# Kernel optimization log

Measured on AMD Instinct MI355X. Metric: run time of the kernel, lower is better.

Reference implementation:

```python
import jax, jax.numpy as jnp
import numpy as np

B, T, C, H = 4, 4096, 1024, 128

def setup_inputs() -> dict:
    key = jax.random.key(0)
    kx, kk, kq, kv = jax.random.split(key, 4)
    x = jax.random.normal(kx, (B, T, C), dtype=jnp.float32)
    # torch nn.Linear(C, H, bias=False) stored here as [C, H] so y = x @ W
    s = 1.0 / np.sqrt(C)
    w_key = jax.random.uniform(kk, (C, H), jnp.float32, -s, s)
    w_query = jax.random.uniform(kq, (C, H), jnp.float32, -s, s)
    w_value = jax.random.uniform(kv, (C, H), jnp.float32, -s, s)
    return {"x": x, "w_key": w_key, "w_query": w_query, "w_value": w_value}

def reference(x, w_key, w_query, w_value):
    # Single-head causal self-attention (dropout p=0.0 -> identity).
    k = x @ w_key      # [B,T,H]
    q = x @ w_query    # [B,T,H]
    v = x @ w_value    # [B,T,H]
    scale = k.shape[-1] ** -0.5
    scores = jnp.einsum('bqh,bkh->bqk', q, k) * scale  # [B,T,T]
    causal = jnp.tril(jnp.ones((x.shape[1], x.shape[1]), dtype=bool))
    scores = jnp.where(causal, scores, -jnp.inf)
    attn = jax.nn.softmax(scores, axis=-1)
    return jnp.einsum('bqk,bkh->bqh', attn, v)  # [B,T,H]
```

## Files before the change

### kernel.cpp

```cpp
#include <hip/hip_runtime.h>
#include <hip/hip_bf16.h>


typedef unsigned short u16;
typedef __attribute__((ext_vector_type(8))) __bf16 bf16x8;
typedef __attribute__((ext_vector_type(8))) u16 u16x8;
typedef __attribute__((ext_vector_type(4))) u16 u16x4;
typedef __attribute__((ext_vector_type(4))) float f32x4;

#define T_DIM 4096
#define C_DIM 1024
#define H_DIM 128
#define EPB 272
#define WS_SPLIT_NEED 50135040ull

static __device__ __forceinline__ f32x4 mfma16x16(u16x8 a, u16x8 b, f32x4 c) {
  return __builtin_amdgcn_mfma_f32_16x16x32_bf16(
      __builtin_bit_cast(bf16x8, a), __builtin_bit_cast(bf16x8, b), c, 0, 0, 0);
}

static __device__ __forceinline__ u16 f2bf(float f) {
  __hip_bfloat16 h = __float2bfloat16(f);
  return __builtin_bit_cast(u16, h);
}

static __device__ __forceinline__ float bf2f(u16 u) {
  unsigned x = (unsigned)u << 16;
  return __builtin_bit_cast(float, x);
}

static __device__ __forceinline__ void gll16(const u16* g, u16* l) {
  __builtin_amdgcn_global_load_lds(
      (const __attribute__((address_space(1))) void*)(void*)g,
      (__attribute__((address_space(3))) void*)l, 16, 0, 0);
}

__global__ __launch_bounds__(256) void prep_w_kernel(
    const float* __restrict__ wk, const float* __restrict__ wq,
    const float* __restrict__ wv, u16* __restrict__ Wf) {
  const int oid = blockIdx.x * 256 + threadIdx.x;
  const int w = oid >> 14;
  const int r = oid & 16383;
  const int nb = r >> 11;
  const int kb = (r >> 6) & 31;
  const int lane = r & 63;
  const int g = lane >> 4, lq = lane & 15;
  const float* W = (w == 0) ? wk : (w == 1) ? wq : wv;
  const float sc = (w == 1) ? 0.08838834764831845f : 1.0f;
  const int k0 = kb * 32 + g * 8;
  const int n = nb * 16 + lq;
  u16x8 o;
#pragma unroll
  for (int j = 0; j < 8; ++j) o[j] = f2bf(W[(size_t)(k0 + j) * H_DIM + n] * sc);
  *(u16x8*)&Wf[(size_t)oid * 8] = o;
}

__global__ __launch_bounds__(512, 2) void proj_kernel(
    const float* __restrict__ x, const u16* __restrict__ Wf,
    u16* __restrict__ Qb, u16* __restrict__ Kb, u16* __restrict__ Vt) {
  __shared__ __attribute__((aligned(16))) u16 smem[32 * 1024];
  const int m0 = blockIdx.x * 32;
  const int t = threadIdx.x;
  const int wave = t >> 6, lane = t & 63;
  const int g = lane >> 4, lq = lane & 15;
  const int lsw = lq & 7;

#pragma unroll
  for (int p = 0; p < 8; ++p) {
    int c = p * 512 + t;
    int row = c >> 7, cc = c & 127;
    const float* xp = &x[(size_t)(m0 + row) * C_DIM + cc * 8];
    float4 v0 = *(const float4*)xp;
    float4 v1 = *(const float4*)(xp + 4);
    u16x8 bv;
    bv[0] = f2bf(v0.x); bv[1] = f2bf(v0.y); bv[2] = f2bf(v0.z); bv[3] = f2bf(v0.w);
    bv[4] = f2bf(v1.x); bv[5] = f2bf(v1.y); bv[6] = f2bf(v1.z); bv[7] = f2bf(v1.w);
    *(u16x8*)&smem[row * 1024 + ((cc ^ (row & 7)) * 8)] = bv;
  }
  __syncthreads();

  f32x4 acc[2][3] = {};
  const u16* wfp[3];
#pragma unroll
  for (int j = 0; j < 3; ++j)
    wfp[j] = &Wf[(size_t)((wave * 3 + j) * 32) * 512 + lane * 8];

  u16x8 bcur[3], bnxt[3];
#pragma unroll
  for (int j = 0; j < 3; ++j) bcur[j] = *(const u16x8*)wfp[j];

  for (int kb = 0; kb < 32; ++kb) {
    const int kn = (kb + 1) & 31;
#pragma unroll
    for (int j = 0; j < 3; ++j)
      bnxt[j] = *(const u16x8*)(wfp[j] + (size_t)kn * 512);
    u16x8 af[2];
#pragma unroll
    for (int i = 0; i < 2; ++i)
      af[i] = *(const u16x8*)&smem[(i * 16 + lq) * 1024 +
                                   (((kb * 4 + g) ^ lsw) * 8)];
#pragma unroll
    for (int i = 0; i < 2; ++i)
#pragma unroll
      for (int j = 0; j < 3; ++j)
        acc[i][j] = mfma16x16(af[i], bcur[j], acc[i][j]);
#pragma unroll
    for (int j = 0; j < 3; ++j) bcur[j] = bnxt[j];
  }

#pragma unroll
  for (int j = 0; j < 3; ++j) {
    const int c384 = wave * 48 + j * 16;
    const int which = c384 >> 7;
    const int col = (c384 & 127) + lq;
    if (which == 0) {
#pragma unroll
      for (int i = 0; i < 2; ++i)
#pragma unroll
        for (int r = 0; r < 4; ++r)
          Kb[(size_t)(m0 + i * 16 + g * 4 + r) * H_DIM + col] =
              f2bf(acc[i][j][r]);
    } else if (which == 1) {
#pragma unroll
      for (int i = 0; i < 2; ++i)
#pragma unroll
        for (int r = 0; r < 4; ++r)
          Qb[(size_t)(m0 + i * 16 + g * 4 + r) * H_DIM + col] =
              f2bf(acc[i][j][r]);
    }
  }
  __syncthreads();
#pragma unroll
  for (int j = 0; j < 3; ++j) {
    const int c384 = wave * 48 + j * 16;
    if ((c384 >> 7) == 2) {
      const int v = (c384 & 127) + lq;
#pragma unroll
      for (int i = 0; i < 2; ++i)
#pragma unroll
        for (int r = 0; r < 4; ++r)
          smem[v * 40 + i * 16 + g * 4 + r] = f2bf(acc[i][j][r]);
    }
  }
  __syncthreads();
  {
    const int b = m0 >> 12;
    const int t0 = m0 & 4095;
    int h = t >> 2, mc = (t & 3) * 8;
    *(u16x8*)&Vt[(size_t)b * (H_DIM * T_DIM) + (size_t)h * T_DIM + t0 + mc] =
        *(const u16x8*)&smem[h * 40 + mc];
  }
}

__global__ __launch_bounds__(512, 4) void attn_kernel(
    const u16* __restrict__ Qb, const u16* __restrict__ Kb,
    const u16* __restrict__ Vt, float* __restrict__ out,
    u16* __restrict__ Opart, float* __restrict__ ml, int split) {
  __shared__ __attribute__((aligned(16))) u16 Kl[64 * 128];
  __shared__ __attribute__((aligned(16))) u16 Vl[128 * 64];
  __shared__ __attribute__((aligned(16))) u16 Pl[8][16 * 72];
  const int t = threadIdx.x;
  const int wave = t >> 6, lane = t & 63;
  const int g = lane >> 4, lq = lane & 15;
  const int lsw = lane & 7;

  int b, qb, kvb, kve, pid;
  if (split) {
    int bid = (int)blockIdx.x;
    int xcd = bid & 7;
    b = xcd >> 1;
    int e = (EPB - 1) - ((bid >> 3) * 2 + (bid & 1));
    int a = 0;
#pragma unroll
    for (int c = 1; c <= 15; ++c)
      if (e >= c * (c + 1)) a = c;
    int off = e - a * (a + 1);
    int d = off / (a + 1);
    int ch = off - d * (a + 1);
    qb = 2 * a + d;
    kvb = ch * 256;
    pid = b * EPB + e;
    int kv_full = qb * 128 + 128;
    kve = (kvb + 256 < kv_full) ? kvb + 256 : kv_full;
  } else {
    b = (int)blockIdx.x & 3;
    qb = 31 - ((int)blockIdx.x >> 2);
    kvb = 0;
    kve = qb * 128 + 128;
    pid = 0;
  }
  const int rowq = qb * 128 + wave * 16;
  const int qrow = rowq + lq;

  u16x8 qf[4];
  {
    const u16* Qp = Qb + (size_t)(b * T_DIM + qrow) * H_DIM;
#pragma unroll
    for (int c = 0; c < 4; ++c) qf[c] = *(const u16x8*)&Qp[c * 32 + g * 8];
  }

  f32x4 ao[8] = {};
  float m_run = -INFINITY, l_run = 0.f;

  const u16* Kg0 = Kb + (size_t)b * T_DIM * H_DIM;
  const u16* Vg0 = Vt + (size_t)b * H_DIM * T_DIM;

  for (int kv0 = kvb; kv0 < kve; kv0 += 64) {
    __syncthreads();
#pragma unroll
    for (int i = 0; i < 2; ++i) {
      int r0 = (i * 8 + wave) * 4;
      int r = r0 + (lane >> 4);
      int csrc = (lane & 15) ^ (r & 7);
      gll16(&Kg0[(size_t)(kv0 + r) * H_DIM + csrc * 8], &Kl[r0 * 128]);
    }
#pragma unroll
    for (int i = 0; i < 2; ++i) {
      int h0 = (i * 8 + wave) * 8;
      int h = h0 + (lane >> 3);
      int csrc = (lane & 7) ^ (lane >> 3);
      gll16(&Vg0[(size_t)h * T_DIM + kv0 + csrc * 8], &Vl[h0 * 64]);
    }
    __syncthreads();

    if (kv0 > rowq + 15) continue;

    f32x4 s[4];
#pragma unroll
    for (int nf = 0; nf < 4; ++nf) s[nf] = f32x4{0.f, 0.f, 0.f, 0.f};
#pragma unroll
    for (int nf = 0; nf < 4; ++nf)
#pragma unroll
      for (int c = 0; c < 4; ++c) {
        u16x8 kf = *(const u16x8*)&Kl[(nf * 16 + lq) * 128 +
                                      (((c * 4 + g) ^ lsw) * 8)];
        s[nf] = mfma16x16(kf, qf[c], s[nf]);
      }

    if (kv0 + 63 > rowq) {
      const int kb = kv0 + g * 4;
#pragma unroll
      for (int nf = 0; nf < 4; ++nf)
#pragma unroll
        for (int r = 0; r < 4; ++r)
          if (kb + nf * 16 + r > qrow) s[nf][r] = -INFINITY;
    }

    float t0 = fmaxf(fmaxf(s[0][0], s[0][1]), fmaxf(s[0][2], s[0][3]));
    float t1 = fmaxf(fmaxf(s[1][0], s[1][1]), fmaxf(s[1][2], s[1][3]));
    float t2 = fmaxf(fmaxf(s[2][0], s[2][1]), fmaxf(s[2][2], s[2][3]));
    float t3 = fmaxf(fmaxf(s[3][0], s[3][1]), fmaxf(s[3][2], s[3][3]));
    float pmax = fmaxf(fmaxf(t0, t1), fmaxf(t2, t3));
    pmax = fmaxf(pmax, __shfl_xor(pmax, 16));
    pmax = fmaxf(pmax, __shfl_xor(pmax, 32));

    float mn = fmaxf(m_run, pmax);
    float al = __expf(m_run - mn);
    m_run = mn;
#pragma unroll
    for (int nf = 0; nf < 4; ++nf)
#pragma unroll
      for (int r = 0; r < 4; ++r) s[nf][r] = __expf(s[nf][r] - mn);
    float u0 = (s[0][0] + s[0][1]) + (s[0][2] + s[0][3]);
    float u1 = (s[1][0] + s[1][1]) + (s[1][2] + s[1][3]);
    float u2 = (s[2][0] + s[2][1]) + (s[2][2] + s[2][3]);
    float u3 = (s[3][0] + s[3][1]) + (s[3][2] + s[3][3]);
    float ps = (u0 + u1) + (u2 + u3);
    ps += __shfl_xor(ps, 16);
    ps += __shfl_xor(ps, 32);
    l_run = l_run * al + ps;

    if (!__all(al == 1.f)) {
      float alr[4];
#pragma unroll
      for (int r = 0; r < 4; ++r) alr[r] = __shfl(al, g * 4 + r);
#pragma unroll
      for (int h8 = 0; h8 < 8; ++h8)
#pragma unroll
        for (int r = 0; r < 4; ++r) ao[h8][r] *= alr[r];
    }

#pragma unroll
    for (int nf = 0; nf < 4; ++nf) {
      u16x4 pw;
#pragma unroll
      for (int r = 0; r < 4; ++r) pw[r] = f2bf(s[nf][r]);
      *(u16x4*)&Pl[wave][lq * 72 + nf * 16 + g * 4] = pw;
    }

    u16x8 pf[2];
#pragma unroll
    for (int kk = 0; kk < 2; ++kk)
      pf[kk] = *(const u16x8*)&Pl[wave][lq * 72 + kk * 32 + g * 8];
#pragma unroll
    for (int h8 = 0; h8 < 8; ++h8)
#pragma unroll
      for (int kk = 0; kk < 2; ++kk) {
        u16x8 vf = *(const u16x8*)&Vl[(h8 * 16 + lq) * 64 +
                                      (((kk * 4 + g) ^ lsw) * 8)];
        ao[h8] = mfma16x16(pf[kk], vf, ao[h8]);
      }
  }

  if (!split) {
    float linv = 1.f / l_run;
    float inv[4];
#pragma unroll
    for (int r = 0; r < 4; ++r) inv[r] = __shfl(linv, g * 4 + r);
    float* Og = out + (size_t)(b * T_DIM + rowq) * H_DIM;
#pragma unroll
    for (int h8 = 0; h8 < 8; ++h8)
#pragma unroll
      for (int r = 0; r < 4; ++r)
        Og[(size_t)(g * 4 + r) * H_DIM + h8 * 16 + lq] = ao[h8][r] * inv[r];
  } else {
    u16* Op = Opart + (size_t)pid * 16384 + (size_t)(wave * 16) * H_DIM;
#pragma unroll
    for (int h8 = 0; h8 < 8; ++h8)
#pragma unroll
      for (int r = 0; r < 4; ++r)
        Op[(g * 4 + r) * H_DIM + h8 * 16 + lq] = f2bf(ao[h8][r]);
    if (lane < 16) {
      float* mlp = ml + (size_t)pid * 256;
      mlp[wave * 16 + lane] = m_run;
      mlp[128 + wave * 16 + lane] = l_run;
    }
  }
}

__global__ __launch_bounds__(256) void combine_kernel(
    const u16* __restrict__ Opart, const float* __restrict__ ml,
    float* __restrict__ out) {
  const int blk = blockIdx.x;
  const int qb = blk >> 2;
  const int sub = blk & 3;
  const int b = blockIdx.y;
  const int t = threadIdx.x;
  const int row = sub * 32 + (t >> 3);
  const int colb = (t & 7) * 16;
  const int a = qb >> 1;
  const int n = a + 1;
  const int base = a * (a + 1) + (qb & 1) * (a + 1);
  const int pid0 = b * EPB + base;

  float M = -INFINITY;
  for (int i = 0; i < n; ++i)
    M = fmaxf(M, ml[(size_t)(pid0 + i) * 256 + row]);

  float L = 0.f;
  float o[16] = {};
  for (int i = 0; i < n; ++i) {
    const size_t mb = (size_t)(pid0 + i) * 256;
    float sc = __expf(ml[mb + row] - M);
    L += sc * ml[mb + 128 + row];
    const u16* Op = Opart + (size_t)(pid0 + i) * 16384 + row * H_DIM + colb;
#pragma unroll
    for (int p = 0; p < 2; ++p) {
      u16x8 v = *(const u16x8*)&Op[p * 8];
#pragma unroll
      for (int e = 0; e < 8; ++e) o[p * 8 + e] += sc * bf2f(v[e]);
    }
  }
  float inv = 1.f / L;
  float* Og = out + ((size_t)b * T_DIM + qb * 128 + row) * H_DIM + colb;
#pragma unroll
  for (int p = 0; p < 4; ++p) {
    f32x4 v = {o[p * 4] * inv, o[p * 4 + 1] * inv, o[p * 4 + 2] * inv,
               o[p * 4 + 3] * inv};
    *(f32x4*)&Og[p * 4] = v;
  }
}

extern "C" void kernel_launch(void* const* d_in, const int* in_sizes, int n_in,
                              void* d_out, int out_size, void* d_ws,
                              size_t ws_size, hipStream_t stream) {
  const float* x = (const float*)d_in[0];
  const float* wk = (const float*)d_in[1];
  const float* wq = (const float*)d_in[2];
  const float* wv = (const float*)d_in[3];
  float* out = (float*)d_out;
  char* ws = (char*)d_ws;

  u16* Wf = (u16*)ws;
  u16* Qb = (u16*)(ws + 786432);
  u16* Kb = (u16*)(ws + 786432 + 4194304);
  u16* Vt = (u16*)(ws + 786432 + 8388608);
  u16* Opart = (u16*)(ws + 13369344);
  float* ml = (float*)(ws + 49020928);

  const int split = (ws_size >= WS_SPLIT_NEED) ? 1 : 0;

  prep_w_kernel<<<192, 256, 0, stream>>>(wk, wq, wv, Wf);
  proj_kernel<<<512, 512, 0, stream>>>(x, Wf, Qb, Kb, Vt);
  if (split) {
    attn_kernel<<<4 * EPB, 512, 0, stream>>>(Qb, Kb, Vt, out, Opart, ml, 1);
    combine_kernel<<<dim3(128, 4), 256, 0, stream>>>(Opart, ml, out);
  } else {
    attn_kernel<<<128, 512, 0, stream>>>(Qb, Kb, Vt, out, Opart, ml, 0);
  }
}
```

Measured before the change: 84.60 us.

## Process 32 query rows per wave with 4-wave blocks to reuse K/V fragments

```diff
diff --git a/kernel.cpp b/kernel.cpp
--- a/kernel.cpp
+++ b/kernel.cpp
@@ -152,13 +152,13 @@
   }
 }
 
-__global__ __launch_bounds__(512, 4) void attn_kernel(
+__global__ __launch_bounds__(256, 3) void attn_kernel(
     const u16* __restrict__ Qb, const u16* __restrict__ Kb,
     const u16* __restrict__ Vt, float* __restrict__ out,
     u16* __restrict__ Opart, float* __restrict__ ml, int split) {
   __shared__ __attribute__((aligned(16))) u16 Kl[64 * 128];
   __shared__ __attribute__((aligned(16))) u16 Vl[128 * 64];
-  __shared__ __attribute__((aligned(16))) u16 Pl[8][16 * 72];
+  __shared__ __attribute__((aligned(16))) u16 Pl[4][32 * 72];
   const int t = threadIdx.x;
   const int wave = t >> 6, lane = t & 63;
   const int g = lane >> 4, lq = lane & 15;
@@ -189,18 +189,18 @@
     kve = qb * 128 + 128;
     pid = 0;
   }
-  const int rowq = qb * 128 + wave * 16;
-  const int qrow = rowq + lq;
-
-  u16x8 qf[4];
-  {
-    const u16* Qp = Qb + (size_t)(b * T_DIM + qrow) * H_DIM;
-#pragma unroll
-    for (int c = 0; c < 4; ++c) qf[c] = *(const u16x8*)&Qp[c * 32 + g * 8];
-  }
-
-  f32x4 ao[8] = {};
-  float m_run = -INFINITY, l_run = 0.f;
+  const int rowq = qb * 128 + wave * 32;
+
+  u16x8 qf[2][4];
+#pragma unroll
+  for (int rf = 0; rf < 2; ++rf) {
+    const u16* Qp = Qb + (size_t)(b * T_DIM + rowq + rf * 16 + lq) * H_DIM;
+#pragma unroll
+    for (int c = 0; c < 4; ++c) qf[rf][c] = *(const u16x8*)&Qp[c * 32 + g * 8];
+  }
+
+  f32x4 ao[2][8] = {};
+  float m_run[2] = {-INFINITY, -INFINITY}, l_run[2] = {0.f, 0.f};
 
   const u16* Kg0 = Kb + (size_t)b * T_DIM * H_DIM;
   const u16* Vg0 = Vt + (size_t)b * H_DIM * T_DIM;
@@ -208,122 +208,157 @@
   for (int kv0 = kvb; kv0 < kve; kv0 += 64) {
     __syncthreads();
 #pragma unroll
-    for (int i = 0; i < 2; ++i) {
-      int r0 = (i * 8 + wave) * 4;
+    for (int i = 0; i < 4; ++i) {
+      int r0 = (i * 4 + wave) * 4;
       int r = r0 + (lane >> 4);
       int csrc = (lane & 15) ^ (r & 7);
       gll16(&Kg0[(size_t)(kv0 + r) * H_DIM + csrc * 8], &Kl[r0 * 128]);
     }
 #pragma unroll
-    for (int i = 0; i < 2; ++i) {
-      int h0 = (i * 8 + wave) * 8;
+    for (int i = 0; i < 4; ++i) {
+      int h0 = (i * 4 + wave) * 8;
       int h = h0 + (lane >> 3);
       int csrc = (lane & 7) ^ (lane >> 3);
       gll16(&Vg0[(size_t)h * T_DIM + kv0 + csrc * 8], &Vl[h0 * 64]);
     }
     __syncthreads();
 
-    if (kv0 > rowq + 15) continue;
-
-    f32x4 s[4];
-#pragma unroll
-    for (int nf = 0; nf < 4; ++nf) s[nf] = f32x4{0.f, 0.f, 0.f, 0.f};
+    if (kv0 > rowq + 31) continue;
+
+    f32x4 s[2][4];
+#pragma unroll
+    for (int rf = 0; rf < 2; ++rf)
+#pragma unroll
+      for (int nf = 0; nf < 4; ++nf) s[rf][nf] = f32x4{0.f, 0.f, 0.f, 0.f};
 #pragma unroll
     for (int nf = 0; nf < 4; ++nf)
 #pragma unroll
       for (int c = 0; c < 4; ++c) {
         u16x8 kf = *(const u16x8*)&Kl[(nf * 16 + lq) * 128 +
                                       (((c * 4 + g) ^ lsw) * 8)];
-        s[nf] = mfma16x16(kf, qf[c], s[nf]);
+#pragma unroll
+        for (int rf = 0; rf < 2; ++rf)
+          s[rf][nf] = mfma16x16(kf, qf[rf][c], s[rf][nf]);
       }
 
     if (kv0 + 63 > rowq) {
       const int kb = kv0 + g * 4;
 #pragma unroll
+      for (int rf = 0; rf < 2; ++rf) {
+        const int qrow = rowq + rf * 16 + lq;
+#pragma unroll
+        for (int nf = 0; nf < 4; ++nf)
+#pragma unroll
+          for (int r = 0; r < 4; ++r)
+            if (kb + nf * 16 + r > qrow) s[rf][nf][r] = -INFINITY;
+      }
+    }
+
+    float al[2];
+#pragma unroll
+    for (int rf = 0; rf < 2; ++rf) {
+      float t0 = fmaxf(fmaxf(s[rf][0][0], s[rf][0][1]),
+                       fmaxf(s[rf][0][2], s[rf][0][3]));
+      float t1 = fmaxf(fmaxf(s[rf][1][0], s[rf][1][1]),
+                       fmaxf(s[rf][1][2], s[rf][1][3]));
+      float t2 = fmaxf(fmaxf(s[rf][2][0], s[rf][2][1]),
+                       fmaxf(s[rf][2][2], s[rf][2][3]));
+      float t3 = fmaxf(fmaxf(s[rf][3][0], s[rf][3][1]),
+                       fmaxf(s[rf][3][2], s[rf][3][3]));
+      float pmax = fmaxf(fmaxf(t0, t1), fmaxf(t2, t3));
+      pmax = fmaxf(pmax, __shfl_xor(pmax, 16));
+      pmax = fmaxf(pmax, __shfl_xor(pmax, 32));
+      float mn = fmaxf(m_run[rf], pmax);
+      al[rf] = __expf(m_run[rf] - mn);
+      m_run[rf] = mn;
+#pragma unroll
       for (int nf = 0; nf < 4; ++nf)
 #pragma unroll
-        for (int r = 0; r < 4; ++r)
-          if (kb + nf * 16 + r > qrow) s[nf][r] = -INFINITY;
-    }
-
-    float t0 = fmaxf(fmaxf(s[0][0], s[0][1]), fmaxf(s[0][2], s[0][3]));
-    float t1 = fmaxf(fmaxf(s[1][0], s[1][1]), fmaxf(s[1][2], s[1][3]));
-    float t2 = fmaxf(fmaxf(s[2][0], s[2][1]), fmaxf(s[2][2], s[2][3]));
-    float t3 = fmaxf(fmaxf(s[3][0], s[3][1]), fmaxf(s[3][2], s[3][3]));
-    float pmax = fmaxf(fmaxf(t0, t1), fmaxf(t2, t3));
-    pmax = fmaxf(pmax, __shfl_xor(pmax, 16));
-    pmax = fmaxf(pmax, __shfl_xor(pmax, 32));
-
-    float mn = fmaxf(m_run, pmax);
-    float al = __expf(m_run - mn);
-    m_run = mn;
-#pragma unroll
-    for (int nf = 0; nf < 4; ++nf)
-#pragma unroll
-      for (int r = 0; r < 4; ++r) s[nf][r] = __expf(s[nf][r] - mn);
-    float u0 = (s[0][0] + s[0][1]) + (s[0][2] + s[0][3]);
-    float u1 = (s[1][0] + s[1][1]) + (s[1][2] + s[1][3]);
-    float u2 = (s[2][0] + s[2][1]) + (s[2][2] + s[2][3]);
-    float u3 = (s[3][0] + s[3][1]) + (s[3][2] + s[3][3]);
-    float ps = (u0 + u1) + (u2 + u3);
-    ps += __shfl_xor(ps, 16);
-    ps += __shfl_xor(ps, 32);
-    l_run = l_run * al + ps;
-
-    if (!__all(al == 1.f)) {
-      float alr[4];
-#pragma unroll
-      for (int r = 0; r < 4; ++r) alr[r] = __shfl(al, g * 4 + r);
-#pragma unroll
-      for (int h8 = 0; h8 < 8; ++h8)
-#pragma unroll
-        for (int r = 0; r < 4; ++r) ao[h8][r] *= alr[r];
-    }
-
-#pragma unroll
-    for (int nf = 0; nf < 4; ++nf) {
-      u16x4 pw;
-#pragma unroll
-      for (int r = 0; r < 4; ++r) pw[r] = f2bf(s[nf][r]);
-      *(u16x4*)&Pl[wave][lq * 72 + nf * 16 + g * 4] = pw;
-    }
-
-    u16x8 pf[2];
-#pragma unroll
-    for (int kk = 0; kk < 2; ++kk)
-      pf[kk] = *(const u16x8*)&Pl[wave][lq * 72 + kk * 32 + g * 8];
+        for (int r = 0; r < 4; ++r) s[rf][nf][r] = __expf(s[rf][nf][r] - mn);
+      float u0 = (s[rf][0][0] + s[rf][0][1]) + (s[rf][0][2] + s[rf][0][3]);
+      float u1 = (s[rf][1][0] + s[rf][1][1]) + (s[rf][1][2] + s[rf][1][3]);
+      float u2 = (s[rf][2][0] + s[rf][2][1]) + (s[rf][2][2] + s[rf][2][3]);
+      float u3 = (s[rf][3][0] + s[rf][3][1]) + (s[rf][3][2] + s[rf][3][3]);
+      float ps = (u0 + u1) + (u2 + u3);
+      ps += __shfl_xor(ps, 16);
+      ps += __shfl_xor(ps, 32);
+      l_run[rf] = l_run[rf] * al[rf] + ps;
+    }
+
+    if (!__all(al[0] == 1.f && al[1] == 1.f)) {
+#pragma unroll
+      for (int rf = 0; rf < 2; ++rf) {
+        float alr[4];
+#pragma unroll
+        for (int r = 0; r < 4; ++r) alr[r] = __shfl(al[rf], g * 4 + r);
+#pragma unroll
+        for (int h8 = 0; h8 < 8; ++h8)
+#pragma unroll
+          for (int r = 0; r < 4; ++r) ao[rf][h8][r] *= alr[r];
+      }
+    }
+
+#pragma unroll
+    for (int rf = 0; rf < 2; ++rf)
+#pragma unroll
+      for (int nf = 0; nf < 4; ++nf) {
+        u16x4 pw;
+#pragma unroll
+        for (int r = 0; r < 4; ++r) pw[r] = f2bf(s[rf][nf][r]);
+        *(u16x4*)&Pl[wave][(rf * 16 + lq) * 72 + nf * 16 + g * 4] = pw;
+      }
+
+    u16x8 pf[2][2];
+#pragma unroll
+    for (int rf = 0; rf < 2; ++rf)
+#pragma unroll
+      for (int kk = 0; kk < 2; ++kk)
+        pf[rf][kk] =
+            *(const u16x8*)&Pl[wave][(rf * 16 + lq) * 72 + kk * 32 + g * 8];
 #pragma unroll
     for (int h8 = 0; h8 < 8; ++h8)
 #pragma unroll
       for (int kk = 0; kk < 2; ++kk) {
         u16x8 vf = *(const u16x8*)&Vl[(h8 * 16 + lq) * 64 +
                                       (((kk * 4 + g) ^ lsw) * 8)];
-        ao[h8] = mfma16x16(pf[kk], vf, ao[h8]);
+#pragma unroll
+        for (int rf = 0; rf < 2; ++rf)
+          ao[rf][h8] = mfma16x16(pf[rf][kk], vf, ao[rf][h8]);
       }
   }
 
   if (!split) {
-    float linv = 1.f / l_run;
-    float inv[4];
-#pragma unroll
-    for (int r = 0; r < 4; ++r) inv[r] = __shfl(linv, g * 4 + r);
-    float* Og = out + (size_t)(b * T_DIM + rowq) * H_DIM;
-#pragma unroll
-    for (int h8 = 0; h8 < 8; ++h8)
-#pragma unroll
-      for (int r = 0; r < 4; ++r)
-        Og[(size_t)(g * 4 + r) * H_DIM + h8 * 16 + lq] = ao[h8][r] * inv[r];
+#pragma unroll
+    for (int rf = 0; rf < 2; ++rf) {
+      float linv = 1.f / l_run[rf];
+      float inv[4];
+#pragma unroll
+      for (int r = 0; r < 4; ++r) inv[r] = __shfl(linv, g * 4 + r);
+      float* Og = out + (size_t)(b * T_DIM + rowq + rf * 16) * H_DIM;
+#pragma unroll
+      for (int h8 = 0; h8 < 8; ++h8)
+#pragma unroll
+        for (int r = 0; r < 4; ++r)
+          Og[(size_t)(g * 4 + r) * H_DIM + h8 * 16 + lq] = ao[rf][h8][r] * inv[r];
+    }
   } else {
-    u16* Op = Opart + (size_t)pid * 16384 + (size_t)(wave * 16) * H_DIM;
-#pragma unroll
-    for (int h8 = 0; h8 < 8; ++h8)
-#pragma unroll
-      for (int r = 0; r < 4; ++r)
-        Op[(g * 4 + r) * H_DIM + h8 * 16 + lq] = f2bf(ao[h8][r]);
+#pragma unroll
+    for (int rf = 0; rf < 2; ++rf) {
+      u16* Op = Opart + (size_t)pid * 16384 +
+                (size_t)(wave * 32 + rf * 16) * H_DIM;
+#pragma unroll
+      for (int h8 = 0; h8 < 8; ++h8)
+#pragma unroll
+        for (int r = 0; r < 4; ++r)
+          Op[(g * 4 + r) * H_DIM + h8 * 16 + lq] = f2bf(ao[rf][h8][r]);
+    }
     if (lane < 16) {
       float* mlp = ml + (size_t)pid * 256;
-      mlp[wave * 16 + lane] = m_run;
-      mlp[128 + wave * 16 + lane] = l_run;
+#pragma unroll
+      for (int rf = 0; rf < 2; ++rf) {
+        mlp[wave * 32 + rf * 16 + lane] = m_run[rf];
+        mlp[128 + wave * 32 + rf * 16 + lane] = l_run[rf];
+      }
     }
   }
 }
@@ -393,9 +428,9 @@
   prep_w_kernel<<<192, 256, 0, stream>>>(wk, wq, wv, Wf);
   proj_kernel<<<512, 512, 0, stream>>>(x, Wf, Qb, Kb, Vt);
   if (split) {
-    attn_kernel<<<4 * EPB, 512, 0, stream>>>(Qb, Kb, Vt, out, Opart, ml, 1);
+    attn_kernel<<<4 * EPB, 256, 0, stream>>>(Qb, Kb, Vt, out, Opart, ml, 1);
     combine_kernel<<<dim3(128, 4), 256, 0, stream>>>(Opart, ml, out);
   } else {
-    attn_kernel<<<128, 512, 0, stream>>>(Qb, Kb, Vt, out, Opart, ml, 0);
-  }
-}
+    attn_kernel<<<128, 256, 0, stream>>>(Qb, Kb, Vt, out, Opart, ml, 0);
+  }
+}
```

After: 98.45 us. 16.4% more time.
